# Performance work log

Hardware: AMD Instinct MI355X
Metric: run time of the kernel (lower is better)

Reference implementation:

```python
import jax, jax.numpy as jnp
import numpy as np

B, H, W, C = 2, 56, 56, 128
DIN, N, R, K = 256, 16, 8, 4   # d_inner, d_state, dt_rank, num scan directions
L = H * W
EPS = 1e-5


def setup_inputs() -> dict:
    ks = jax.random.split(jax.random.key(0), 10)
    def p(i, shape, scale=0.02):
        return jax.random.normal(ks[i], shape, jnp.float32) * scale
    x = jax.random.normal(ks[0], (B, H, W, C), jnp.float32)
    # A_log init as in mamba: log(1..N) tiled over K*DIN channels
    A_logs = jnp.log(jnp.tile(jnp.arange(1, N + 1, dtype=jnp.float32)[None, :], (K * DIN, 1)))
    return {
        "x": x,
        "in_proj_w": p(1, (2 * DIN, C)),
        "in_proj_b": jnp.zeros((2 * DIN,), jnp.float32),
        "conv_w": p(2, (DIN, 1, 3, 3), 0.1),   # depthwise 3x3
        "conv_b": jnp.zeros((DIN,), jnp.float32),
        "x_proj_w": p(3, (K, R + 2 * N, DIN)),
        "dt_projs_w": p(4, (K, DIN, R), 0.1),
        "dt_projs_b": p(5, (K, DIN), 0.1),
        "A_logs": A_logs,
        "Ds": jnp.ones((K * DIN,), jnp.float32),
        "out_norm_w": jnp.ones((DIN,), jnp.float32),
        "out_norm_b": jnp.zeros((DIN,), jnp.float32),
        "out_proj_w": p(6, (C, DIN)),
        "out_proj_b": jnp.zeros((C,), jnp.float32),
    }


def _silu(v):
    return v * jax.nn.sigmoid(v)


def _ss2d(x, in_proj_w, in_proj_b, conv_w, conv_b, x_proj_w, dt_projs_w,
          dt_projs_b, A_logs, Ds, out_norm_w, out_norm_b, out_proj_w, out_proj_b):
    # ---- input projection + gate ----
    xz = jnp.einsum('bhwc,ec->bhwe', x, in_proj_w) + in_proj_b  # [B,H,W,2*DIN]
    xh, z = xz[..., :DIN], xz[..., DIN:]
    z = _silu(z)
    # ---- depthwise conv (channel-first) + act ----
    xc = jnp.transpose(xh, (0, 3, 1, 2))  # [B,DIN,H,W]
    xc = jax.lax.conv_general_dilated(xc, conv_w, (1, 1), ((1, 1), (1, 1)),
                                      feature_group_count=DIN)
    xc = _silu(xc + conv_b[None, :, None, None])
    # ---- cross scan (scans=0): [id, transpose, flip(id), flip(transpose)] ----
    x0 = xc.reshape(B, DIN, L)
    x1 = jnp.transpose(xc, (0, 1, 3, 2)).reshape(B, DIN, L)
    xs = jnp.stack([x0, x1, x0[..., ::-1], x1[..., ::-1]], axis=1)  # [B,K,DIN,L]
    # ---- x_proj -> (dt, B, C), dt_proj ----
    x_dbl = jnp.einsum('bkdl,kcd->bkcl', xs, x_proj_w)
    dts, Bs, Cs = x_dbl[:, :, :R], x_dbl[:, :, R:R + N], x_dbl[:, :, R + N:]
    dts = jnp.einsum('bkrl,kdr->bkdl', dts, dt_projs_w)
    delta = jax.nn.softplus(dts + dt_projs_b[None, :, :, None])  # [B,K,DIN,L]
    A = -jnp.exp(A_logs).reshape(K, DIN, N)
    # ---- selective scan over L (time-major) ----
    u_t = jnp.transpose(xs, (3, 0, 1, 2))     # [L,B,K,DIN]
    d_t = jnp.transpose(delta, (3, 0, 1, 2))  # [L,B,K,DIN]
    B_t = jnp.transpose(Bs, (3, 0, 1, 2))     # [L,B,K,N]
    C_t = jnpp = jnp.transpose(Cs, (3, 0, 1, 2))

    def step(state, inp):
        u_i, d_i, b_i, c_i = inp
        dA = jnp.exp(d_i[..., None] * A)                       # [B,K,DIN,N]
        state = dA * state + (d_i * u_i)[..., None] * b_i[:, :, None, :]
        y = jnp.einsum('bkdn,bkn->bkd', state, c_i)
        return state, y

    state0 = jnp.zeros((B, K, DIN, N), jnp.float32)
    _, ys = jax.lax.scan(step, state0, (u_t, d_t, B_t, C_t))   # ys: [L,B,K,DIN]
    ys = jnp.transpose(ys, (1, 2, 3, 0))                       # [B,K,DIN,L]
    ys = ys + xs * Ds.reshape(1, K, DIN, 1)
    # ---- cross merge (scans=0) ----
    y01 = ys[:, 0:2] + ys[:, 2:4][..., ::-1]                   # [B,2,DIN,L]
    y = y01[:, 0] + jnp.transpose(y01[:, 1].reshape(B, DIN, W, H), (0, 1, 3, 2)).reshape(B, DIN, L)
    y = jnp.transpose(y.reshape(B, DIN, H, W), (0, 2, 3, 1))   # [B,H,W,DIN]
    # ---- out_norm (LayerNorm over DIN), gate, out_proj ----
    mu = jnp.mean(y, axis=-1, keepdims=True)
    var = jnp.mean((y - mu) ** 2, axis=-1, keepdims=True)
    y = (y - mu) / jnp.sqrt(var + EPS) * out_norm_w + out_norm_b
    y = y * z
    return jnp.einsum('bhwd,cd->bhwc', y, out_proj_w) + out_proj_b


def reference(x, in_proj_w, in_proj_b, conv_w, conv_b, x_proj_w, dt_projs_w,
              dt_projs_b, A_logs, Ds, out_norm_w, out_norm_b, out_proj_w, out_proj_b):
    return _ss2d(x, in_proj_w, in_proj_b, conv_w, conv_b, x_proj_w, dt_projs_w,
                 dt_projs_b, A_logs, Ds, out_norm_w, out_norm_b, out_proj_w, out_proj_b)
```

## Files before the change

### kernel.cpp

```cpp
#include <hip/hip_runtime.h>

#define B_  2
#define H_  56
#define W_  56
#define C_  128
#define DIN 256
#define NS  16
#define RR  8
#define KK  4
#define LL  3136
#define CD  40
#define PC  98
#define LC  32

#define WOFF_Z     0
#define WOFF_XC    1605632
#define WOFF_XDBL  3211264
#define WOFF_SEND  4214784
#define WOFF_DSUM  7426048
#define WOFF_YDIR  7626752
#define WOFF_XBF   14049280
#define WOFF_IPWBF 14450688
#define WOFF_OPWBF 14483456

typedef __attribute__((ext_vector_type(8))) short bf16x8;
typedef __attribute__((ext_vector_type(4))) float f32x4;

__device__ __forceinline__ unsigned short f2bf(float f){
    unsigned int u = __float_as_uint(f);
    u += 0x7fffu + ((u >> 16) & 1u);
    return (unsigned short)(u >> 16);
}
__device__ __forceinline__ float siluf(float x){ return x / (1.f + __expf(-x)); }

__device__ __forceinline__ int sidx(int k, int l){
    int j = (k < 2) ? l : (LL - 1 - l);
    if ((k & 1) == 0) return j;
    return (j % H_) * W_ + (j / H_);
}

__global__ __launch_bounds__(256) void k_prep(
        const float* __restrict__ x, const float* __restrict__ ipw,
        const float* __restrict__ opw,
        unsigned short* __restrict__ xbf, unsigned short* __restrict__ ipwbf,
        unsigned short* __restrict__ opwbf){
    int g4 = (blockIdx.x*256 + threadIdx.x)*4;
    const float* src; unsigned short* dst; int off;
    if (g4 < 802816){ src = x; dst = xbf; off = g4; }
    else if (g4 < 868352){ src = ipw; dst = ipwbf; off = g4 - 802816; }
    else { src = opw; dst = opwbf; off = g4 - 868352; }
    float4 v = *reinterpret_cast<const float4*>(src + off);
    uint2 pk;
    pk.x = (unsigned int)f2bf(v.x) | ((unsigned int)f2bf(v.y) << 16);
    pk.y = (unsigned int)f2bf(v.z) | ((unsigned int)f2bf(v.w) << 16);
    *reinterpret_cast<uint2*>(dst + off) = pk;
}

__global__ __launch_bounds__(256) void k_gemm_in(
        const unsigned short* __restrict__ xbf,
        const unsigned short* __restrict__ ipwbf,
        const float* __restrict__ ipb,
        float* __restrict__ xh, float* __restrict__ z){
    int nt = blockIdx.x & 7, mt = blockIdx.x >> 3;
    int t = threadIdx.x;
    int w = t >> 6, lane = t & 63;
    int r = lane & 15, q = lane >> 4;
    int m0 = mt*64 + w*16;
    int n0 = nt*64;
    f32x4 acc[4];
    #pragma unroll
    for (int i = 0; i < 4; ++i) acc[i] = (f32x4){0.f,0.f,0.f,0.f};
    const unsigned short* arow = xbf + (size_t)(m0 + r)*128 + q*8;
    #pragma unroll
    for (int ks = 0; ks < 4; ++ks){
        bf16x8 a = *reinterpret_cast<const bf16x8*>(arow + ks*32);
        #pragma unroll
        for (int tt = 0; tt < 4; ++tt){
            bf16x8 b = *reinterpret_cast<const bf16x8*>(
                ipwbf + (size_t)(n0 + tt*16 + r)*128 + ks*32 + q*8);
            acc[tt] = __builtin_amdgcn_mfma_f32_16x16x32_bf16(a, b, acc[tt], 0,0,0);
        }
    }
    #pragma unroll
    for (int tt = 0; tt < 4; ++tt){
        int col = n0 + tt*16 + r;
        float bias = ipb[col];
        #pragma unroll
        for (int reg = 0; reg < 4; ++reg){
            int row = m0 + q*4 + reg;
            float v = acc[tt][reg] + bias;
            if (nt < 4) xh[(size_t)row*DIN + col] = v;
            else        z[(size_t)row*DIN + (col - DIN)] = siluf(v);
        }
    }
}

#define CSPLIT 4
#define CCOLS  14
__global__ __launch_bounds__(256) void k_conv(
        const float* __restrict__ cw, const float* __restrict__ cb,
        const float* __restrict__ xh, float* __restrict__ xc){
    int bi = blockIdx.x;
    int sw = bi & 3; int h = (bi >> 2) % H_; int b = bi / (H_*CSPLIT);
    int d = threadIdx.x;
    float cwv[9];
    #pragma unroll
    for (int i = 0; i < 9; ++i) cwv[i] = cw[d*9 + i];
    float bias = cb[d];
    const float* base[3];
    bool rv[3];
    #pragma unroll
    for (int i = 0; i < 3; ++i){
        int nh = h - 1 + i;
        rv[i] = (nh >= 0 && nh < H_);
        base[i] = xh + ((size_t)b*LL + (rv[i] ? nh : 0)*W_)*DIN + d;
    }
    int w0 = sw*CCOLS;
    float a0,a1,a2, b0,b1,b2, c0,c1,c2;
    a0 = (w0 > 0 && rv[0]) ? base[0][(w0-1)*DIN] : 0.f;
    a1 = (w0 > 0 && rv[1]) ? base[1][(w0-1)*DIN] : 0.f;
    a2 = (w0 > 0 && rv[2]) ? base[2][(w0-1)*DIN] : 0.f;
    b0 = rv[0] ? base[0][w0*DIN] : 0.f;
    b1 = rv[1] ? base[1][w0*DIN] : 0.f;
    b2 = rv[2] ? base[2][w0*DIN] : 0.f;
    for (int w = w0; w < w0 + CCOLS; ++w){
        bool cin = (w + 1 < W_);
        c0 = (cin && rv[0]) ? base[0][(w+1)*DIN] : 0.f;
        c1 = (cin && rv[1]) ? base[1][(w+1)*DIN] : 0.f;
        c2 = (cin && rv[2]) ? base[2][(w+1)*DIN] : 0.f;
        float acc = bias;
        acc = fmaf(a0, cwv[0], acc); acc = fmaf(b0, cwv[1], acc); acc = fmaf(c0, cwv[2], acc);
        acc = fmaf(a1, cwv[3], acc); acc = fmaf(b1, cwv[4], acc); acc = fmaf(c1, cwv[5], acc);
        acc = fmaf(a2, cwv[6], acc); acc = fmaf(b2, cwv[7], acc); acc = fmaf(c2, cwv[8], acc);
        xc[((size_t)b*LL + h*W_ + w)*DIN + d] = siluf(acc);
        a0=b0; a1=b1; a2=b2; b0=c0; b1=c1; b2=c2;
    }
}

__global__ __launch_bounds__(256) void k_gemm_xp(
        const float* __restrict__ xpw, const float* __restrict__ xc,
        float* __restrict__ xdbl){
    __shared__ __align__(16) float As[128*64];
    __shared__ __align__(16) float Bs[128*49];
    int bi = blockIdx.x;
    int lt = bi % 49; int dir = (bi / 49) & 3; int b = bi / 196;
    int t = threadIdx.x;
    const float4* X4 = reinterpret_cast<const float4*>(xc);
    const float4* W4 = reinterpret_cast<const float4*>(xpw);
    int tm = t & 15, tn = t >> 4;
    float acc[4][3];
    #pragma unroll
    for (int i = 0; i < 4; ++i){ acc[i][0]=0.f; acc[i][1]=0.f; acc[i][2]=0.f; }

    for (int kc = 0; kc < 2; ++kc){
        int m = t & 63, kkb = (t >> 6) * 8;
        int l = lt*64 + m;
        int srow = b*LL + sidx(dir, l);
        #pragma unroll
        for (int j = 0; j < 8; ++j){
            int kk = kkb + j;
            float4 va = X4[(size_t)srow*64 + kc*32 + kk];
            As[(kk*4+0)*64 + m] = va.x; As[(kk*4+1)*64 + m] = va.y;
            As[(kk*4+2)*64 + m] = va.z; As[(kk*4+3)*64 + m] = va.w;
            if (m < CD){
                float4 vb = W4[((size_t)dir*CD + m)*64 + kc*32 + kk];
                Bs[(kk*4+0)*49 + m] = vb.x; Bs[(kk*4+1)*49 + m] = vb.y;
                Bs[(kk*4+2)*49 + m] = vb.z; Bs[(kk*4+3)*49 + m] = vb.w;
            } else if (m < 48){
                Bs[(kk*4+0)*49 + m] = 0.f; Bs[(kk*4+1)*49 + m] = 0.f;
                Bs[(kk*4+2)*49 + m] = 0.f; Bs[(kk*4+3)*49 + m] = 0.f;
            }
        }
        __syncthreads();
        #pragma unroll 8
        for (int k = 0; k < 128; ++k){
            float4 av = *reinterpret_cast<const float4*>(As + k*64 + tm*4);
            float b0 = Bs[k*49 + tn*3 + 0];
            float b1 = Bs[k*49 + tn*3 + 1];
            float b2 = Bs[k*49 + tn*3 + 2];
            acc[0][0]=fmaf(av.x,b0,acc[0][0]); acc[0][1]=fmaf(av.x,b1,acc[0][1]); acc[0][2]=fmaf(av.x,b2,acc[0][2]);
            acc[1][0]=fmaf(av.y,b0,acc[1][0]); acc[1][1]=fmaf(av.y,b1,acc[1][1]); acc[1][2]=fmaf(av.y,b2,acc[1][2]);
            acc[2][0]=fmaf(av.z,b0,acc[2][0]); acc[2][1]=fmaf(av.z,b1,acc[2][1]); acc[2][2]=fmaf(av.z,b2,acc[2][2]);
            acc[3][0]=fmaf(av.w,b0,acc[3][0]); acc[3][1]=fmaf(av.w,b1,acc[3][1]); acc[3][2]=fmaf(av.w,b2,acc[3][2]);
        }
        __syncthreads();
    }
    size_t orow = ((size_t)(b*KK + dir)*LL + lt*64);
    #pragma unroll
    for (int i = 0; i < 4; ++i){
        int lrow = tm*4 + i;
        #pragma unroll
        for (int j = 0; j < 3; ++j){
            int n = tn*3 + j;
            if (n < CD) xdbl[(orow + lrow)*CD + n] = acc[i][j];
        }
    }
}

__global__ __launch_bounds__(128) void k_scanA(
        const float* __restrict__ dtw_, const float* __restrict__ dtb_,
        const float* __restrict__ alg,
        const float* __restrict__ xc, const float* __restrict__ xdbl,
        float* __restrict__ send, float* __restrict__ dsum){
    int id = blockIdx.x >> 1;
    int dh = blockIdx.x & 1;
    int c = id % PC; int bk = id / PC; int k = bk % KK; int b = bk / KK;
    int d = dh*128 + threadIdx.x;
    const float4* xr = reinterpret_cast<const float4*>(xdbl + (size_t)id*LC*CD);

    float dtw[RR];
    #pragma unroll
    for (int r = 0; r < RR; ++r) dtw[r] = dtw_[(k*DIN + d)*RR + r];
    float dtb = dtb_[k*DIN + d];
    float aa[NS];
    #pragma unroll
    for (int n = 0; n < NS; ++n) aa[n] = -__expf(alg[(k*DIN + d)*NS + n]);
    float st[NS];
    #pragma unroll
    for (int n = 0; n < NS; ++n) st[n] = 0.f;
    float cum = 0.f;
    const float* xcb = xc + (size_t)b*LL*DIN + d;

    for (int l = 0; l < LC; ++l){
        float4 q0 = xr[l*10+0], q1 = xr[l*10+1];
        float xdt = dtb;
        xdt = fmaf(q0.x, dtw[0], xdt); xdt = fmaf(q0.y, dtw[1], xdt);
        xdt = fmaf(q0.z, dtw[2], xdt); xdt = fmaf(q0.w, dtw[3], xdt);
        xdt = fmaf(q1.x, dtw[4], xdt); xdt = fmaf(q1.y, dtw[5], xdt);
        xdt = fmaf(q1.z, dtw[6], xdt); xdt = fmaf(q1.w, dtw[7], xdt);
        float delta = (xdt > 15.f) ? xdt : __logf(1.f + __expf(xdt));
        cum += delta;
        float u = xcb[(size_t)sidx(k, c*LC + l)*DIN];
        float du = delta * u;
        float4 B0 = xr[l*10+2], B1 = xr[l*10+3], B2 = xr[l*10+4], B3 = xr[l*10+5];
        float bv[NS] = {B0.x,B0.y,B0.z,B0.w, B1.x,B1.y,B1.z,B1.w,
                        B2.x,B2.y,B2.z,B2.w, B3.x,B3.y,B3.z,B3.w};
        #pragma unroll
        for (int n = 0; n < NS; ++n){
            float dA = __expf(delta * aa[n]);
            st[n] = fmaf(dA, st[n], du * bv[n]);
        }
    }
    float4* so = reinterpret_cast<float4*>(send + ((size_t)id*DIN + d)*NS);
    #pragma unroll
    for (int n4 = 0; n4 < 4; ++n4)
        so[n4] = make_float4(st[n4*4], st[n4*4+1], st[n4*4+2], st[n4*4+3]);
    dsum[id*DIN + d] = cum;
}

__global__ __launch_bounds__(256) void k_comb(
        const float* __restrict__ alg,
        float* __restrict__ send, const float* __restrict__ dsum){
    int gid = blockIdx.x*256 + threadIdx.x;
    int n = gid & 15; int d = (gid >> 4) & 255; int bk = gid >> 12;
    int k = bk & 3;
    float A = -__expf(alg[(k*DIN + d)*NS + n]);
    const size_t cstr = (size_t)DIN*NS;
    float* sp = send + ((size_t)bk*PC*DIN + d)*NS + n;
    const float* dp = dsum + (size_t)bk*PC*DIN + d;
    float s_c = sp[0];
    float d_c = dp[0];
    float init = 0.f;
    for (int c = 0; c < PC; ++c){
        float s_n = 0.f, d_n = 0.f;
        if (c + 1 < PC){ s_n = sp[(size_t)(c+1)*cstr]; d_n = dp[(c+1)*DIN]; }
        sp[(size_t)c*cstr] = init;
        init = fmaf(__expf(d_c * A), init, s_c);
        s_c = s_n; d_c = d_n;
    }
}

__global__ __launch_bounds__(128) void k_scanB(
        const float* __restrict__ dtw_, const float* __restrict__ dtb_,
        const float* __restrict__ alg, const float* __restrict__ dss,
        const float* __restrict__ xc, const float* __restrict__ xdbl,
        const float* __restrict__ sinit, float* __restrict__ ydir){
    int id = blockIdx.x >> 1;
    int dh = blockIdx.x & 1;
    int c = id % PC; int bk = id / PC; int k = bk % KK; int b = bk / KK;
    int d = dh*128 + threadIdx.x;
    const float4* xr = reinterpret_cast<const float4*>(xdbl + (size_t)id*LC*CD);

    float dtw[RR];
    #pragma unroll
    for (int r = 0; r < RR; ++r) dtw[r] = dtw_[(k*DIN + d)*RR + r];
    float dtb = dtb_[k*DIN + d];
    float Dd  = dss[k*DIN + d];
    float aa[NS];
    #pragma unroll
    for (int n = 0; n < NS; ++n) aa[n] = -__expf(alg[(k*DIN + d)*NS + n]);
    float st[NS];
    const float4* si = reinterpret_cast<const float4*>(sinit + ((size_t)id*DIN + d)*NS);
    #pragma unroll
    for (int n4 = 0; n4 < 4; ++n4){
        float4 v = si[n4];
        st[n4*4] = v.x; st[n4*4+1] = v.y; st[n4*4+2] = v.z; st[n4*4+3] = v.w;
    }
    const float* xcb = xc + (size_t)b*LL*DIN + d;
    float* yo = ydir + ((size_t)bk*LL + c*LC)*DIN + d;

    for (int l = 0; l < LC; ++l){
        float4 q0 = xr[l*10+0], q1 = xr[l*10+1];
        float xdt = dtb;
        xdt = fmaf(q0.x, dtw[0], xdt); xdt = fmaf(q0.y, dtw[1], xdt);
        xdt = fmaf(q0.z, dtw[2], xdt); xdt = fmaf(q0.w, dtw[3], xdt);
        xdt = fmaf(q1.x, dtw[4], xdt); xdt = fmaf(q1.y, dtw[5], xdt);
        xdt = fmaf(q1.z, dtw[6], xdt); xdt = fmaf(q1.w, dtw[7], xdt);
        float delta = (xdt > 15.f) ? xdt : __logf(1.f + __expf(xdt));
        float u = xcb[(size_t)sidx(k, c*LC + l)*DIN];
        float du = delta * u;
        float4 B0 = xr[l*10+2], B1 = xr[l*10+3], B2 = xr[l*10+4], B3 = xr[l*10+5];
        float4 C0 = xr[l*10+6], C1 = xr[l*10+7], C2 = xr[l*10+8], C3 = xr[l*10+9];
        float bv[NS] = {B0.x,B0.y,B0.z,B0.w, B1.x,B1.y,B1.z,B1.w,
                        B2.x,B2.y,B2.z,B2.w, B3.x,B3.y,B3.z,B3.w};
        float cv[NS] = {C0.x,C0.y,C0.z,C0.w, C1.x,C1.y,C1.z,C1.w,
                        C2.x,C2.y,C2.z,C2.w, C3.x,C3.y,C3.z,C3.w};
        float yv = Dd * u;
        #pragma unroll
        for (int n = 0; n < NS; ++n){
            float dA = __expf(delta * aa[n]);
            st[n] = fmaf(dA, st[n], du * bv[n]);
            yv = fmaf(st[n], cv[n], yv);
        }
        yo[(size_t)l*DIN] = yv;
    }
}

__global__ __launch_bounds__(256) void k_ln(
        const float* __restrict__ onw, const float* __restrict__ onb,
        const float* __restrict__ ydir, const float* __restrict__ z,
        unsigned short* __restrict__ ynbf){
    int bl = blockIdx.x;
    int b = bl / LL; int s = bl % LL;
    int t = threadIdx.x;
    int h = s / W_, w = s % W_;
    int l1 = w*H_ + h;
    size_t base = (size_t)b*KK*LL;
    float v = ydir[(base + 0*LL + s)         *DIN + t]
            + ydir[(base + 1*LL + l1)        *DIN + t]
            + ydir[(base + 2*LL + (LL-1-s))  *DIN + t]
            + ydir[(base + 3*LL + (LL-1-l1)) *DIN + t];
    __shared__ float red[8];
    float s1 = v, s2 = v*v;
    #pragma unroll
    for (int o = 32; o > 0; o >>= 1){
        s1 += __shfl_down(s1, o);
        s2 += __shfl_down(s2, o);
    }
    if ((t & 63) == 0){ red[t >> 6] = s1; red[4 + (t >> 6)] = s2; }
    __syncthreads();
    float sum  = red[0] + red[1] + red[2] + red[3];
    float sumq = red[4] + red[5] + red[6] + red[7];
    float mu = sum * (1.f/DIN);
    float var = fmaxf(sumq * (1.f/DIN) - mu*mu, 0.f);
    float rstd = rsqrtf(var + 1e-5f);
    float yn = ((v - mu) * rstd * onw[t] + onb[t]) * z[(size_t)bl*DIN + t];
    ynbf[(size_t)bl*DIN + t] = f2bf(yn);
}

__global__ __launch_bounds__(128) void k_gemm_out(
        const unsigned short* __restrict__ ynbf,
        const unsigned short* __restrict__ opwbf,
        const float* __restrict__ opb, float* __restrict__ out){
    int mt = blockIdx.x;
    int t = threadIdx.x;
    int w = t >> 6, lane = t & 63;
    int r = lane & 15, q = lane >> 4;
    int m0 = mt*16;
    int n0 = w*64;
    f32x4 acc[4];
    #pragma unroll
    for (int i = 0; i < 4; ++i) acc[i] = (f32x4){0.f,0.f,0.f,0.f};
    const unsigned short* arow = ynbf + (size_t)(m0 + r)*256 + q*8;
    #pragma unroll
    for (int ks = 0; ks < 8; ++ks){
        bf16x8 a = *reinterpret_cast<const bf16x8*>(arow + ks*32);
        #pragma unroll
        for (int tt = 0; tt < 4; ++tt){
            bf16x8 b = *reinterpret_cast<const bf16x8*>(
                opwbf + (size_t)(n0 + tt*16 + r)*256 + ks*32 + q*8);
            acc[tt] = __builtin_amdgcn_mfma_f32_16x16x32_bf16(a, b, acc[tt], 0,0,0);
        }
    }
    #pragma unroll
    for (int tt = 0; tt < 4; ++tt){
        int col = n0 + tt*16 + r;
        float bias = opb[col];
        #pragma unroll
        for (int reg = 0; reg < 4; ++reg){
            int row = m0 + q*4 + reg;
            out[(size_t)row*C_ + col] = acc[tt][reg] + bias;
        }
    }
}

extern "C" void kernel_launch(void* const* d_in, const int* in_sizes, int n_in,
                              void* d_out, int out_size, void* d_ws, size_t ws_size,
                              hipStream_t stream){
    const float* x   = (const float*)d_in[0];
    const float* ipw = (const float*)d_in[1];
    const float* ipb = (const float*)d_in[2];
    const float* cw  = (const float*)d_in[3];
    const float* cb  = (const float*)d_in[4];
    const float* xpw = (const float*)d_in[5];
    const float* dtw = (const float*)d_in[6];
    const float* dtb = (const float*)d_in[7];
    const float* alg = (const float*)d_in[8];
    const float* dss = (const float*)d_in[9];
    const float* onw = (const float*)d_in[10];
    const float* onb = (const float*)d_in[11];
    const float* opw = (const float*)d_in[12];
    const float* opb = (const float*)d_in[13];

    float* ws   = (float*)d_ws;
    float* z    = ws + WOFF_Z;
    float* xc   = ws + WOFF_XC;
    float* xdbl = ws + WOFF_XDBL;
    float* send = ws + WOFF_SEND;
    float* dsum = ws + WOFF_DSUM;
    float* ydir = ws + WOFF_YDIR;
    float* xh   = ws + WOFF_YDIR;
    unsigned short* xbf   = (unsigned short*)(ws + WOFF_XBF);
    unsigned short* ipwbf = (unsigned short*)(ws + WOFF_IPWBF);
    unsigned short* opwbf = (unsigned short*)(ws + WOFF_OPWBF);
    unsigned short* ynbf  = (unsigned short*)(ws + WOFF_XC);

    k_prep    <<<880, 256, 0, stream>>>(x, ipw, opw, xbf, ipwbf, opwbf);
    k_gemm_in <<<98*8, 256, 0, stream>>>(xbf, ipwbf, ipb, xh, z);
    k_conv    <<<B_*H_*CSPLIT, 256, 0, stream>>>(cw, cb, xh, xc);
    k_gemm_xp <<<B_*KK*49, 256, 0, stream>>>(xpw, xc, xdbl);
    k_scanA   <<<B_*KK*PC*2, 128, 0, stream>>>(dtw, dtb, alg, xc, xdbl, send, dsum);
    k_comb    <<<(B_*KK*DIN*NS)/256, 256, 0, stream>>>(alg, send, dsum);
    k_scanB   <<<B_*KK*PC*2, 128, 0, stream>>>(dtw, dtb, alg, dss, xc, xdbl, send, ydir);
    k_ln      <<<B_*LL, 256, 0, stream>>>(onw, onb, ydir, z, ynbf);
    k_gemm_out<<<392, 128, 0, stream>>>(ynbf, opwbf, opb, (float*)d_out);
}
```

Baseline: 231.8 us.

## Run x_proj GEMM on bf16 MFMA with conv emitting bf16 activations

The x_proj GEMM moves from an fp32 shared-memory FMA kernel to bf16 MFMA 16x16x32 instructions. The conv kernel now also writes a bf16 copy of its activations, and the prep kernel converts x_proj weights to bf16, padded from 40 to 48 rows per direction. The conv is split into 8 column chunks instead of 4 to launch more blocks. In exchange, the extra bf16 store adds write traffic, and dt/B/C are computed at lower precision.

```diff
diff --git a/kernel.cpp b/kernel.cpp
--- a/kernel.cpp
+++ b/kernel.cpp
@@ -22,6 +22,8 @@
 #define WOFF_XBF   14049280
 #define WOFF_IPWBF 14450688
 #define WOFF_OPWBF 14483456
+#define WOFF_XPWBF 14499840
+#define WOFF_XCBF  14524416
 
 typedef __attribute__((ext_vector_type(8))) short bf16x8;
 typedef __attribute__((ext_vector_type(4))) float f32x4;
@@ -41,15 +43,29 @@
 
 __global__ __launch_bounds__(256) void k_prep(
         const float* __restrict__ x, const float* __restrict__ ipw,
-        const float* __restrict__ opw,
+        const float* __restrict__ opw, const float* __restrict__ xpw,
         unsigned short* __restrict__ xbf, unsigned short* __restrict__ ipwbf,
-        unsigned short* __restrict__ opwbf){
+        unsigned short* __restrict__ opwbf, unsigned short* __restrict__ xpwbf){
     int g4 = (blockIdx.x*256 + threadIdx.x)*4;
-    const float* src; unsigned short* dst; int off;
-    if (g4 < 802816){ src = x; dst = xbf; off = g4; }
-    else if (g4 < 868352){ src = ipw; dst = ipwbf; off = g4 - 802816; }
-    else { src = opw; dst = opwbf; off = g4 - 868352; }
-    float4 v = *reinterpret_cast<const float4*>(src + off);
+    if (g4 >= 950272) return;
+    float4 v;
+    unsigned short* dst; int off;
+    if (g4 < 802816){
+        off = g4; dst = xbf;
+        v = *reinterpret_cast<const float4*>(x + off);
+    } else if (g4 < 868352){
+        off = g4 - 802816; dst = ipwbf;
+        v = *reinterpret_cast<const float4*>(ipw + off);
+    } else if (g4 < 901120){
+        off = g4 - 868352; dst = opwbf;
+        v = *reinterpret_cast<const float4*>(opw + off);
+    } else {
+        off = g4 - 901120; dst = xpwbf;
+        int dir = off / 12288; int rem = off % 12288;
+        int row = rem >> 8;    int col = rem & 255;
+        if (row < CD) v = *reinterpret_cast<const float4*>(xpw + ((size_t)dir*CD + row)*256 + col);
+        else          v = make_float4(0.f, 0.f, 0.f, 0.f);
+    }
     uint2 pk;
     pk.x = (unsigned int)f2bf(v.x) | ((unsigned int)f2bf(v.y) << 16);
     pk.y = (unsigned int)f2bf(v.z) | ((unsigned int)f2bf(v.w) << 16);
@@ -95,13 +111,14 @@
     }
 }
 
-#define CSPLIT 4
-#define CCOLS  14
+#define CSPLIT 8
+#define CCOLS  7
 __global__ __launch_bounds__(256) void k_conv(
         const float* __restrict__ cw, const float* __restrict__ cb,
-        const float* __restrict__ xh, float* __restrict__ xc){
+        const float* __restrict__ xh, float* __restrict__ xc,
+        unsigned short* __restrict__ xcbf){
     int bi = blockIdx.x;
-    int sw = bi & 3; int h = (bi >> 2) % H_; int b = bi / (H_*CSPLIT);
+    int sw = bi & 7; int h = (bi >> 3) % H_; int b = bi / (H_*CSPLIT);
     int d = threadIdx.x;
     float cwv[9];
     #pragma unroll
@@ -132,67 +149,47 @@
         acc = fmaf(a0, cwv[0], acc); acc = fmaf(b0, cwv[1], acc); acc = fmaf(c0, cwv[2], acc);
         acc = fmaf(a1, cwv[3], acc); acc = fmaf(b1, cwv[4], acc); acc = fmaf(c1, cwv[5], acc);
         acc = fmaf(a2, cwv[6], acc); acc = fmaf(b2, cwv[7], acc); acc = fmaf(c2, cwv[8], acc);
-        xc[((size_t)b*LL + h*W_ + w)*DIN + d] = siluf(acc);
+        float s = siluf(acc);
+        size_t idx = ((size_t)b*LL + h*W_ + w)*DIN + d;
+        xc[idx] = s;
+        xcbf[idx] = f2bf(s);
         a0=b0; a1=b1; a2=b2; b0=c0; b1=c1; b2=c2;
     }
 }
 
 __global__ __launch_bounds__(256) void k_gemm_xp(
-        const float* __restrict__ xpw, const float* __restrict__ xc,
+        const unsigned short* __restrict__ xcbf,
+        const unsigned short* __restrict__ xpwbf,
         float* __restrict__ xdbl){
-    __shared__ __align__(16) float As[128*64];
-    __shared__ __align__(16) float Bs[128*49];
     int bi = blockIdx.x;
     int lt = bi % 49; int dir = (bi / 49) & 3; int b = bi / 196;
     int t = threadIdx.x;
-    const float4* X4 = reinterpret_cast<const float4*>(xc);
-    const float4* W4 = reinterpret_cast<const float4*>(xpw);
-    int tm = t & 15, tn = t >> 4;
-    float acc[4][3];
-    #pragma unroll
-    for (int i = 0; i < 4; ++i){ acc[i][0]=0.f; acc[i][1]=0.f; acc[i][2]=0.f; }
-
-    for (int kc = 0; kc < 2; ++kc){
-        int m = t & 63, kkb = (t >> 6) * 8;
-        int l = lt*64 + m;
-        int srow = b*LL + sidx(dir, l);
-        #pragma unroll
-        for (int j = 0; j < 8; ++j){
-            int kk = kkb + j;
-            float4 va = X4[(size_t)srow*64 + kc*32 + kk];
-            As[(kk*4+0)*64 + m] = va.x; As[(kk*4+1)*64 + m] = va.y;
-            As[(kk*4+2)*64 + m] = va.z; As[(kk*4+3)*64 + m] = va.w;
-            if (m < CD){
-                float4 vb = W4[((size_t)dir*CD + m)*64 + kc*32 + kk];
-                Bs[(kk*4+0)*49 + m] = vb.x; Bs[(kk*4+1)*49 + m] = vb.y;
-                Bs[(kk*4+2)*49 + m] = vb.z; Bs[(kk*4+3)*49 + m] = vb.w;
-            } else if (m < 48){
-                Bs[(kk*4+0)*49 + m] = 0.f; Bs[(kk*4+1)*49 + m] = 0.f;
-                Bs[(kk*4+2)*49 + m] = 0.f; Bs[(kk*4+3)*49 + m] = 0.f;
-            }
-        }
-        __syncthreads();
-        #pragma unroll 8
-        for (int k = 0; k < 128; ++k){
-            float4 av = *reinterpret_cast<const float4*>(As + k*64 + tm*4);
-            float b0 = Bs[k*49 + tn*3 + 0];
-            float b1 = Bs[k*49 + tn*3 + 1];
-            float b2 = Bs[k*49 + tn*3 + 2];
-            acc[0][0]=fmaf(av.x,b0,acc[0][0]); acc[0][1]=fmaf(av.x,b1,acc[0][1]); acc[0][2]=fmaf(av.x,b2,acc[0][2]);
-            acc[1][0]=fmaf(av.y,b0,acc[1][0]); acc[1][1]=fmaf(av.y,b1,acc[1][1]); acc[1][2]=fmaf(av.y,b2,acc[1][2]);
-            acc[2][0]=fmaf(av.z,b0,acc[2][0]); acc[2][1]=fmaf(av.z,b1,acc[2][1]); acc[2][2]=fmaf(av.z,b2,acc[2][2]);
-            acc[3][0]=fmaf(av.w,b0,acc[3][0]); acc[3][1]=fmaf(av.w,b1,acc[3][1]); acc[3][2]=fmaf(av.w,b2,acc[3][2]);
-        }
-        __syncthreads();
-    }
-    size_t orow = ((size_t)(b*KK + dir)*LL + lt*64);
-    #pragma unroll
-    for (int i = 0; i < 4; ++i){
-        int lrow = tm*4 + i;
-        #pragma unroll
-        for (int j = 0; j < 3; ++j){
-            int n = tn*3 + j;
-            if (n < CD) xdbl[(orow + lrow)*CD + n] = acc[i][j];
+    int w = t >> 6, lane = t & 63;
+    int r = lane & 15, q = lane >> 4;
+    int m0 = lt*64 + w*16;
+    int srow = b*LL + sidx(dir, m0 + r);
+    const unsigned short* arow = xcbf + (size_t)srow*DIN + q*8;
+    f32x4 acc[3];
+    #pragma unroll
+    for (int i = 0; i < 3; ++i) acc[i] = (f32x4){0.f,0.f,0.f,0.f};
+    #pragma unroll
+    for (int ks = 0; ks < 8; ++ks){
+        bf16x8 a = *reinterpret_cast<const bf16x8*>(arow + ks*32);
+        #pragma unroll
+        for (int tt = 0; tt < 3; ++tt){
+            bf16x8 bfrag = *reinterpret_cast<const bf16x8*>(
+                xpwbf + ((size_t)dir*48 + tt*16 + r)*DIN + ks*32 + q*8);
+            acc[tt] = __builtin_amdgcn_mfma_f32_16x16x32_bf16(a, bfrag, acc[tt], 0,0,0);
+        }
+    }
+    size_t obase = (size_t)(b*KK + dir)*LL + m0 + q*4;
+    #pragma unroll
+    for (int tt = 0; tt < 3; ++tt){
+        int col = tt*16 + r;
+        if (col < CD){
+            #pragma unroll
+            for (int reg = 0; reg < 4; ++reg)
+                xdbl[(obase + reg)*CD + col] = acc[tt][reg];
         }
     }
 }
@@ -423,12 +420,14 @@
     unsigned short* xbf   = (unsigned short*)(ws + WOFF_XBF);
     unsigned short* ipwbf = (unsigned short*)(ws + WOFF_IPWBF);
     unsigned short* opwbf = (unsigned short*)(ws + WOFF_OPWBF);
+    unsigned short* xpwbf = (unsigned short*)(ws + WOFF_XPWBF);
+    unsigned short* xcbf  = (unsigned short*)(ws + WOFF_XCBF);
     unsigned short* ynbf  = (unsigned short*)(ws + WOFF_XC);
 
-    k_prep    <<<880, 256, 0, stream>>>(x, ipw, opw, xbf, ipwbf, opwbf);
+    k_prep    <<<928, 256, 0, stream>>>(x, ipw, opw, xpw, xbf, ipwbf, opwbf, xpwbf);
     k_gemm_in <<<98*8, 256, 0, stream>>>(xbf, ipwbf, ipb, xh, z);
-    k_conv    <<<B_*H_*CSPLIT, 256, 0, stream>>>(cw, cb, xh, xc);
-    k_gemm_xp <<<B_*KK*49, 256, 0, stream>>>(xpw, xc, xdbl);
+    k_conv    <<<B_*H_*CSPLIT, 256, 0, stream>>>(cw, cb, xh, xc, xcbf);
+    k_gemm_xp <<<B_*KK*49, 256, 0, stream>>>(xcbf, xpwbf, xdbl);
     k_scanA   <<<B_*KK*PC*2, 128, 0, stream>>>(dtw, dtb, alg, xc, xdbl, send, dsum);
     k_comb    <<<(B_*KK*DIN*NS)/256, 256, 0, stream>>>(alg, send, dsum);
     k_scanB   <<<B_*KK*PC*2, 128, 0, stream>>>(dtw, dtb, alg, dss, xc, xdbl, send, ydir);
```

Result: faster. 212.4 us (-8.4%).
